# Optimization experiments

Measured on AMD Instinct MI355X. Metric: run time of the kernel, lower is better.

The kernel has to match this reference:

```python
import jax, jax.numpy as jnp
import numpy as np

BATCH, SEQ = 1, 2048
D_MODEL, N_HEADS, D_HEAD = 2048, 16, 128
ROTARY_DIM = 128
N_CTX = 2048
EPS = 1e-5
IGNORE = -100000.0
ATTN_SCALE = float(np.sqrt(D_HEAD))  # use_attn_scale=True, no layer-idx scaling
ROTARY_BASE = 10000.0


def _ln_pre(x):
    # LayerNormPre: center and normalize, no learned scale/bias
    x = x - x.mean(axis=-1, keepdims=True)
    scale = jnp.sqrt((x * x).mean(axis=-1, keepdims=True) + EPS)
    return x / scale


def _sin_cos_rotary(rotary_dim, n_ctx, base=ROTARY_BASE):
    pos = jnp.arange(n_ctx, dtype=jnp.float32)
    dim = jnp.arange(rotary_dim // 2, dtype=jnp.float32)
    freq = base ** (dim / (rotary_dim / 2))
    freq = jnp.repeat(freq, 2)  # einops.repeat 'd -> (d 2)' (interleaved)
    angles = pos[:, None] / freq[None, :]  # [n_ctx, rotary_dim]
    return jnp.sin(angles), jnp.cos(angles)


def _rotate_every_two(x):
    x1 = x[..., 0::2]
    x2 = x[..., 1::2]
    return jnp.stack([-x2, x1], axis=-1).reshape(x.shape)


def _apply_rotary(x, sin, cos):
    # x: [batch, pos, head, d_head]
    n_pos = x.shape[1]
    x_rot = x[..., :ROTARY_DIM]
    x_pass = x[..., ROTARY_DIM:]
    c = cos[:n_pos][:, None, :]  # [pos, 1, rotary_dim] broadcasts over head
    s = sin[:n_pos][:, None, :]
    x_rotated = x_rot * c + _rotate_every_two(x_rot) * s
    return jnp.concatenate([x_rotated, x_pass], axis=-1)


def setup_inputs() -> dict:
    key = jax.random.key(0)
    ks = jax.random.split(key, 6)
    init_std = 0.02
    return {
        "resid_pre": jax.random.normal(ks[0], (BATCH, SEQ, D_MODEL), jnp.float32),
        "W_Q": jax.random.normal(ks[1], (N_HEADS, D_MODEL, D_HEAD), jnp.float32) * init_std,
        "W_K": jax.random.normal(ks[2], (N_HEADS, D_MODEL, D_HEAD), jnp.float32) * init_std,
        "W_V": jax.random.normal(ks[3], (N_HEADS, D_MODEL, D_HEAD), jnp.float32) * init_std,
        "W_O": jax.random.normal(ks[4], (N_HEADS, D_HEAD, D_MODEL), jnp.float32) * init_std,
        "b_Q": jnp.zeros((N_HEADS, D_HEAD), jnp.float32),
        "b_K": jnp.zeros((N_HEADS, D_HEAD), jnp.float32),
        "b_V": jnp.zeros((N_HEADS, D_HEAD), jnp.float32),
        "b_O": jnp.zeros((D_MODEL,), jnp.float32),
    }


def reference(resid_pre, W_Q, W_K, W_V, W_O, b_Q, b_K, b_V, b_O):
    sin, cos = _sin_cos_rotary(ROTARY_DIM, N_CTX)
    xn = _ln_pre(resid_pre)  # LayerNormPre applied to resid_pre for q, k, v
    q = jnp.einsum("bpd,hde->bphe", xn, W_Q) + b_Q
    k = jnp.einsum("bpd,hde->bphe", xn, W_K) + b_K
    v = jnp.einsum("bpd,hde->bphe", xn, W_V) + b_V
    q = _apply_rotary(q, sin, cos)
    k = _apply_rotary(k, sin, cos)
    # attn_scores: [batch, head, query_pos, key_pos]
    scores = jnp.einsum("bqhe,bkhe->bhqk", q, k) / ATTN_SCALE
    n_pos = resid_pre.shape[1]
    causal = jnp.tril(jnp.ones((n_pos, n_pos), dtype=bool))
    scores = jnp.where(causal, scores, jnp.float32(IGNORE))
    attn = jax.nn.softmax(scores, axis=-1)
    z = jnp.einsum("bkhe,bhqk->bqhe", v, attn)
    out = jnp.einsum("bqhe,hed->bqd", z, W_O) + b_O
    return out
```

## Files before the change

### kernel.cpp

```cpp
#include <hip/hip_runtime.h>
#include <hip/hip_bf16.h>

#define SEQ    2048
#define DM     2048
#define NH     16
#define DH     128
#define EPS    1e-5f
#define SCALE_INV 0.08838834764831845f
#define SC2LOG    0.12751744995f

typedef unsigned short u16;
typedef u16  u16x4  __attribute__((ext_vector_type(4)));
typedef u16  u16x8  __attribute__((ext_vector_type(8)));
typedef __bf16 bf16x8 __attribute__((ext_vector_type(8)));
typedef float f32x4 __attribute__((ext_vector_type(4)));

__device__ __forceinline__ u16 f2bf(float f) {
    unsigned int u = __builtin_bit_cast(unsigned int, f);
    u += 0x7fffu + ((u >> 16) & 1u);
    return (u16)(u >> 16);
}
__device__ __forceinline__ float bf2f(u16 v) {
    return __builtin_bit_cast(float, (unsigned)v << 16);
}
__device__ __forceinline__ bf16x8 as_bf(u16x8 v) { return __builtin_bit_cast(bf16x8, v); }

__device__ __forceinline__ void gload16(const u16* g, u16* l) {
    __builtin_amdgcn_global_load_lds(
        (const __attribute__((address_space(1))) unsigned int*)g,
        (__attribute__((address_space(3))) unsigned int*)l, 16, 0, 0);
}

#define VMCNT(N) asm volatile("s_waitcnt vmcnt(" #N ")" ::: "memory")
#define LGKMCNT0 asm volatile("s_waitcnt lgkmcnt(0)" ::: "memory")
#define SCHEDBAR __builtin_amdgcn_sched_barrier(0)
#define BARRIER  __builtin_amdgcn_s_barrier()

__global__ void rope_kernel(float2* __restrict__ tab) {
    int i = threadIdx.x;
    int pos = blockIdx.x;
    float freq = powf(10000.f, (float)i * (1.f / 64.f));
    float ang = (float)pos / freq;
    tab[pos * 64 + i] = make_float2(sinf(ang), cosf(ang));
}

__global__ __launch_bounds__(256) void ln_kernel(const float* __restrict__ x,
                                                 u16* __restrict__ xn) {
    int row = blockIdx.x, t = threadIdx.x;
    const float* xr = x + (size_t)row * DM;
    float4 v0 = *(const float4*)(xr + t * 4);
    float4 v1 = *(const float4*)(xr + 1024 + t * 4);
    float s = v0.x + v0.y + v0.z + v0.w + v1.x + v1.y + v1.z + v1.w;
    float q = v0.x*v0.x + v0.y*v0.y + v0.z*v0.z + v0.w*v0.w
            + v1.x*v1.x + v1.y*v1.y + v1.z*v1.z + v1.w*v1.w;
    #pragma unroll
    for (int o = 32; o; o >>= 1) { s += __shfl_xor(s, o); q += __shfl_xor(q, o); }
    __shared__ float ss[4], qq[4];
    if ((t & 63) == 0) { ss[t >> 6] = s; qq[t >> 6] = q; }
    __syncthreads();
    s = ss[0] + ss[1] + ss[2] + ss[3];
    q = qq[0] + qq[1] + qq[2] + qq[3];
    float mean = s * (1.f / DM);
    float var  = q * (1.f / DM) - mean * mean;
    float rstd = rsqrtf(var + EPS);
    u16* orow = xn + (size_t)row * DM;
    u16x4 o0 = { f2bf((v0.x-mean)*rstd), f2bf((v0.y-mean)*rstd),
                 f2bf((v0.z-mean)*rstd), f2bf((v0.w-mean)*rstd) };
    u16x4 o1 = { f2bf((v1.x-mean)*rstd), f2bf((v1.y-mean)*rstd),
                 f2bf((v1.z-mean)*rstd), f2bf((v1.w-mean)*rstd) };
    *(u16x4*)(orow + t * 4) = o0;
    *(u16x4*)(orow + 1024 + t * 4) = o1;
}

__global__ __launch_bounds__(256) void transpose_qkv(const float* __restrict__ WQ,
                                                     const float* __restrict__ WK,
                                                     const float* __restrict__ WV,
                                                     u16* __restrict__ out) {
    int z = blockIdx.z, which = z >> 4, h = z & 15;
    const float* in = ((which == 0) ? WQ : (which == 1) ? WK : WV) + (size_t)h * DM * DH;
    u16* o = out + (size_t)z * DM * DH;
    int r0 = blockIdx.y * 64, c0 = blockIdx.x * 64;
    __shared__ u16 tile[64][65];
    int t = threadIdx.x;
    #pragma unroll
    for (int it = 0; it < 4; ++it) {
        int idx = t + it * 256;
        int rr = idx >> 4, cc = (idx & 15) * 4;
        float4 v = *(const float4*)(in + (size_t)(r0 + rr) * DH + c0 + cc);
        tile[rr][cc+0] = f2bf(v.x); tile[rr][cc+1] = f2bf(v.y);
        tile[rr][cc+2] = f2bf(v.z); tile[rr][cc+3] = f2bf(v.w);
    }
    __syncthreads();
    #pragma unroll
    for (int it = 0; it < 4; ++it) {
        int idx = t + it * 256;
        int oc = idx >> 4, orr = (idx & 15) * 4;
        u16x4 w = { tile[orr+0][oc], tile[orr+1][oc], tile[orr+2][oc], tile[orr+3][oc] };
        *(u16x4*)(o + (size_t)(c0 + oc) * DM + r0 + orr) = w;
    }
}

__global__ __launch_bounds__(256) void transpose_wo(const float* __restrict__ in,
                                                    u16* __restrict__ out) {
    int r0 = blockIdx.y * 64, c0 = blockIdx.x * 64;
    __shared__ u16 tile[64][65];
    int t = threadIdx.x;
    #pragma unroll
    for (int it = 0; it < 4; ++it) {
        int idx = t + it * 256;
        int rr = idx >> 4, cc = (idx & 15) * 4;
        float4 v = *(const float4*)(in + (size_t)(r0 + rr) * DM + c0 + cc);
        tile[rr][cc+0] = f2bf(v.x); tile[rr][cc+1] = f2bf(v.y);
        tile[rr][cc+2] = f2bf(v.z); tile[rr][cc+3] = f2bf(v.w);
    }
    __syncthreads();
    #pragma unroll
    for (int it = 0; it < 4; ++it) {
        int idx = t + it * 256;
        int oc = idx >> 4, orr = (idx & 15) * 4;
        u16x4 w = { tile[orr+0][oc], tile[orr+1][oc], tile[orr+2][oc], tile[orr+3][oc] };
        *(u16x4*)(out + (size_t)(c0 + oc) * DM + r0 + orr) = w;
    }
}

__global__ __launch_bounds__(512, 2) void gemm_qkv(const u16* __restrict__ Xn,
                                                   const u16* __restrict__ Wt,
                                                   const float* __restrict__ bQ,
                                                   const float* __restrict__ bK,
                                                   const float* __restrict__ bV,
                                                   const float2* __restrict__ rope,
                                                   u16* __restrict__ qkv) {
    __shared__ u16 As[2][256 * 64], Bs[2][256 * 64];
    int id = blockIdx.x;
    int swz = (id & 7) * 24 + (id >> 3);
    int bx = swz & 7, by = swz >> 3;
    int m0 = bx * 256, n0 = by * 256;

    int t = threadIdx.x, lane = t & 63, wid = t >> 6;
    int wr = wid >> 2, wc = wid & 3;
    int cl = lane & 15, g = lane >> 4;

    auto stage = [&](int buf, int kt) {
        const u16* xa = Xn + (size_t)kt * 64;
        const u16* xb = Wt + (size_t)kt * 64;
        #pragma unroll
        for (int j = 0; j < 4; ++j) {
            int idx = t + j * 512;
            int row = idx >> 3;
            int slotS = (idx & 7) ^ (row & 7);
            gload16(xa + (size_t)(m0 + row) * DM + slotS * 8, &As[buf][idx * 8]);
            gload16(xb + (size_t)(n0 + row) * DM + slotS * 8, &Bs[buf][idx * 8]);
        }
    };

    f32x4 acc[8][4] = {};
    stage(0, 0);
    VMCNT(0);
    BARRIER;

    for (int kt = 0; kt < 32; ++kt) {
        int p = kt & 1;
        bool more = (kt + 1 < 32);
        bf16x8 bfr[4][2], af[4][2];
        #pragma unroll
        for (int nj = 0; nj < 4; ++nj)
            #pragma unroll
            for (int kk = 0; kk < 2; ++kk) {
                int row = wc * 64 + nj * 16 + cl;
                int s = (kk * 4 + g) ^ (row & 7);
                bfr[nj][kk] = as_bf(*(const u16x8*)&Bs[p][row * 64 + s * 8]);
            }
        #pragma unroll
        for (int mi = 0; mi < 4; ++mi)
            #pragma unroll
            for (int kk = 0; kk < 2; ++kk) {
                int row = wr * 128 + mi * 16 + cl;
                int s = (kk * 4 + g) ^ (row & 7);
                af[mi][kk] = as_bf(*(const u16x8*)&As[p][row * 64 + s * 8]);
            }
        if (more) stage(p ^ 1, kt + 1);
        __builtin_amdgcn_s_setprio(1);
        #pragma unroll
        for (int mi = 0; mi < 4; ++mi)
            #pragma unroll
            for (int nj = 0; nj < 4; ++nj)
                #pragma unroll
                for (int kk = 0; kk < 2; ++kk)
                    acc[mi][nj] = __builtin_amdgcn_mfma_f32_16x16x32_bf16(af[mi][kk], bfr[nj][kk], acc[mi][nj], 0, 0, 0);
        __builtin_amdgcn_s_setprio(0);
        #pragma unroll
        for (int mi = 0; mi < 4; ++mi)
            #pragma unroll
            for (int kk = 0; kk < 2; ++kk) {
                int row = wr * 128 + 64 + mi * 16 + cl;
                int s = (kk * 4 + g) ^ (row & 7);
                af[mi][kk] = as_bf(*(const u16x8*)&As[p][row * 64 + s * 8]);
            }
        __builtin_amdgcn_s_setprio(1);
        #pragma unroll
        for (int mi = 0; mi < 4; ++mi)
            #pragma unroll
            for (int nj = 0; nj < 4; ++nj)
                #pragma unroll
                for (int kk = 0; kk < 2; ++kk)
                    acc[4 + mi][nj] = __builtin_amdgcn_mfma_f32_16x16x32_bf16(af[mi][kk], bfr[nj][kk], acc[4 + mi][nj], 0, 0, 0);
        __builtin_amdgcn_s_setprio(0);
        VMCNT(0);
        SCHEDBAR;
        BARRIER;
    }

    int which = n0 >> 11;
    const float* bias = (which == 0) ? bQ : (which == 1) ? bK : bV;
    #pragma unroll
    for (int i = 0; i < 8; ++i)
        #pragma unroll
        for (int nj = 0; nj < 4; ++nj) {
            int eg = n0 + wc * 64 + nj * 16 + cl;
            int h = (eg >> 7) & 15;
            int e = eg & 127;
            float bb = bias[h * DH + e];
            int p0 = m0 + wr * 128 + i * 16 + g * 4;
            if (which == 2) {
                u16* vbase = qkv + 2ll * NH * SEQ * DH + (size_t)h * DH * SEQ;
                u16x4 o = { f2bf(acc[i][nj][0] + bb), f2bf(acc[i][nj][1] + bb),
                            f2bf(acc[i][nj][2] + bb), f2bf(acc[i][nj][3] + bb) };
                *(u16x4*)(vbase + (size_t)e * SEQ + p0) = o;
            } else {
                u16* outbase = qkv + ((size_t)which * 16 + h) * SEQ * DH;
                #pragma unroll
                for (int r = 0; r < 4; ++r) {
                    int pp = p0 + r;
                    float v = acc[i][nj][r] + bb;
                    float pv = __shfl_xor(v, 1);
                    float2 sc2 = rope[pp * 64 + (e >> 1)];
                    v = (e & 1) ? (v * sc2.y + pv * sc2.x) : (v * sc2.y - pv * sc2.x);
                    outbase[(size_t)pp * DH + e] = f2bf(v);
                }
            }
        }
}

__device__ __forceinline__ int part_prefix(int j) {
    return (j < 16) ? 2 * (j - 8) : (j < 24 ? 16 + 3 * (j - 16) : 40 + 4 * (j - 24));
}

__global__ __launch_bounds__(256) void flash_kernel(const u16* __restrict__ Qg,
                                                    const u16* __restrict__ Kg,
                                                    const u16* __restrict__ Vt,
                                                    u16* __restrict__ Zg,
                                                    u16* __restrict__ pO,
                                                    float2* __restrict__ ml) {
    __shared__ u16 kt[64 * 128];
    __shared__ u16 vt[128 * 64];
    __shared__ unsigned pt32[4 * 16 * 32];
    int h = blockIdx.x;
    int rem = blockIdx.y;
    int j = 31, c = 0;
    #pragma unroll 1
    for (int jj = 31; jj >= 0; --jj) {
        int ncj = (jj >> 3) + 1;
        if (rem < ncj) { j = jj; c = rem; break; }
        rem -= ncj;
    }
    int q0 = j * 64;
    int nc = (j >> 3) + 1;
    bool multi = (nc > 1);
    int kt0 = c * 8;
    int kt1 = min(j, c * 8 + 7);

    int t = threadIdx.x, lane = t & 63, w = t >> 6;
    int cl = lane & 15, g = lane >> 4;
    int qw0 = q0 + w * 16;
    const size_t hs = (size_t)h * SEQ;
    unsigned* ptw = pt32 + w * (16 * 32) + cl * 32;
    int swv = (cl & 7) << 1;

    bf16x8 qf[4];
    #pragma unroll
    for (int st = 0; st < 4; ++st)
        qf[st] = as_bf(*(const u16x8*)(Qg + (hs + qw0 + cl) * DH + st * 32 + g * 8));

    f32x4 acc[8] = {};
    float mrun = -3e38f, lsum = 0.f;

    u16x8 kreg[4], vreg[4];
    auto load_tile = [&](int kv0) {
        #pragma unroll
        for (int jj = 0; jj < 4; ++jj) {
            int idx = t + jj * 256;
            kreg[jj] = *(const u16x8*)(Kg + (hs + kv0 + (idx >> 4)) * DH + (idx & 15) * 8);
            vreg[jj] = *(const u16x8*)(Vt + ((size_t)h * DH + (idx >> 3)) * SEQ + kv0 + (idx & 7) * 8);
        }
    };
    auto store_tile = [&]() {
        #pragma unroll
        for (int jj = 0; jj < 4; ++jj) {
            int idx = t + jj * 256;
            int row = idx >> 4, slot = idx & 15;
            *(u16x8*)((char*)kt + row * 256 + ((slot ^ (row & 7)) * 16)) = kreg[jj];
            int e = idx >> 3, ch = idx & 7;
            *(u16x8*)((char*)vt + e * 128 + ((ch ^ (e & 7)) * 16)) = vreg[jj];
        }
    };

    int kvbeg = kt0 * 64, kvend = kt1 * 64;
    load_tile(kvbeg);
    store_tile();

    for (int kv0 = kvbeg; kv0 <= kvend; kv0 += 64) {
        __syncthreads();
        bool more = (kv0 + 64 <= kvend);
        if (more) load_tile(kv0 + 64);

        f32x4 sc[4] = {};
        __builtin_amdgcn_s_setprio(1);
        #pragma unroll
        for (int st = 0; st < 4; ++st)
            #pragma unroll
            for (int cc = 0; cc < 4; ++cc) {
                int row = cc * 16 + cl;
                bf16x8 kf = as_bf(*(const u16x8*)((char*)kt + row * 256 + (((st * 4 + g) ^ (row & 7)) * 16)));
                sc[cc] = __builtin_amdgcn_mfma_f32_16x16x32_bf16(kf, qf[st], sc[cc], 0, 0, 0);
            }
        __builtin_amdgcn_s_setprio(0);

        bool needmask = (kv0 + 63 > qw0);
        int qrow = qw0 + cl;
        float pf[4][4];
        float tm = -3e38f;
        #pragma unroll
        for (int cc = 0; cc < 4; ++cc)
            #pragma unroll
            for (int r = 0; r < 4; ++r) {
                int kvq = kv0 + cc * 16 + g * 4 + r;
                float sval = sc[cc][r] * SC2LOG;
                if (needmask) sval = (kvq <= qrow) ? sval : -3e38f;
                pf[cc][r] = sval;
                tm = fmaxf(tm, sval);
            }
        tm = fmaxf(tm, __shfl_xor(tm, 16));
        tm = fmaxf(tm, __shfl_xor(tm, 32));

        if (!__all(tm <= mrun + 12.f)) {
            float mn = fmaxf(mrun, tm);
            float alpha = exp2f(mrun - mn);
            mrun = mn;
            lsum *= alpha;
            float aR[4];
            #pragma unroll
            for (int r = 0; r < 4; ++r) aR[r] = __shfl(alpha, g * 4 + r);
            #pragma unroll
            for (int n = 0; n < 8; ++n)
                #pragma unroll
                for (int r = 0; r < 4; ++r) acc[n][r] *= aR[r];
        }
        float rs = 0.f;
        #pragma unroll
        for (int cc = 0; cc < 4; ++cc)
            #pragma unroll
            for (int r = 0; r < 4; ++r) {
                float e2 = exp2f(pf[cc][r] - mrun);
                pf[cc][r] = e2;
                rs += e2;
            }
        rs += __shfl_xor(rs, 16);
        rs += __shfl_xor(rs, 32);
        lsum += rs;

        #pragma unroll
        for (int cc = 0; cc < 4; ++cc) {
            unsigned lo = (unsigned)f2bf(pf[cc][0]) | ((unsigned)f2bf(pf[cc][1]) << 16);
            unsigned hi = (unsigned)f2bf(pf[cc][2]) | ((unsigned)f2bf(pf[cc][3]) << 16);
            int u = (cc * 4 + g) ^ swv;
            *(unsigned long long*)(ptw + u * 2) =
                (unsigned long long)lo | ((unsigned long long)hi << 32);
        }
        bf16x8 pa[2];
        #pragma unroll
        for (int ks = 0; ks < 2; ++ks)
            pa[ks] = as_bf(*(const u16x8*)(ptw + ((ks * 8 + g * 2) ^ swv) * 2));

        __builtin_amdgcn_s_setprio(1);
        #pragma unroll
        for (int n = 0; n < 8; ++n)
            #pragma unroll
            for (int ks = 0; ks < 2; ++ks) {
                int e = n * 16 + cl;
                bf16x8 vf = as_bf(*(const u16x8*)((char*)vt + e * 128 + (((ks * 4 + g) ^ (e & 7)) * 16)));
                acc[n] = __builtin_amdgcn_mfma_f32_16x16x32_bf16(pa[ks], vf, acc[n], 0, 0, 0);
            }
        __builtin_amdgcn_s_setprio(0);

        if (!more) break;
        __syncthreads();
        store_tile();
    }

    if (multi) {
        int pidx = h * 72 + part_prefix(j) + c;
        if (lane < 16) ml[(size_t)pidx * 64 + w * 16 + cl] = make_float2(mrun, lsum);
        u16* po = pO + (size_t)pidx * (64 * 128);
        #pragma unroll
        for (int n = 0; n < 8; ++n)
            #pragma unroll
            for (int r = 0; r < 4; ++r)
                po[(w * 16 + g * 4 + r) * 128 + n * 16 + cl] = f2bf(acc[n][r]);
    } else {
        float inv = 1.0f / lsum;
        float invR[4];
        #pragma unroll
        for (int r = 0; r < 4; ++r) invR[r] = __shfl(inv, g * 4 + r);
        #pragma unroll
        for (int n = 0; n < 8; ++n)
            #pragma unroll
            for (int r = 0; r < 4; ++r) {
                int q = qw0 + g * 4 + r;
                Zg[(hs + q) * DH + n * 16 + cl] = f2bf(acc[n][r] * invR[r]);
            }
    }
}

__global__ __launch_bounds__(256) void merge_kernel(const u16* __restrict__ pO,
                                                    const float2* __restrict__ ml,
                                                    u16* __restrict__ Zg) {
    int h = blockIdx.x;
    int j = blockIdx.y + 8;
    int nc = (j >> 3) + 1;
    int pbase = h * 72 + part_prefix(j);
    int t = threadIdx.x;
    int row = t >> 2;
    int c0 = (t & 3) * 32;

    float mv[4], lv[4];
    float M = -3e38f;
    #pragma unroll
    for (int i = 0; i < 4; ++i) {
        int ii = (i < nc) ? i : 0;
        float2 mli = ml[(size_t)(pbase + ii) * 64 + row];
        mv[i] = mli.x; lv[i] = mli.y;
        if (i < nc) M = fmaxf(M, mli.x);
    }
    float wgt[4];
    float L = 0.f;
    #pragma unroll
    for (int i = 0; i < 4; ++i) {
        wgt[i] = (i < nc) ? exp2f(mv[i] - M) : 0.f;
        L += wgt[i] * lv[i];
    }
    float invL = 1.f / L;

    #pragma unroll
    for (int ccc = 0; ccc < 32; ccc += 8) {
        float o[8] = {};
        #pragma unroll
        for (int i = 0; i < 4; ++i) {
            int ii = (i < nc) ? i : 0;
            u16x8 v = *(const u16x8*)(pO + ((size_t)(pbase + ii) * 64 + row) * 128 + c0 + ccc);
            #pragma unroll
            for (int k = 0; k < 8; ++k) o[k] += wgt[i] * bf2f(v[k]);
        }
        u16x8 zv;
        #pragma unroll
        for (int k = 0; k < 8; ++k) zv[k] = f2bf(o[k] * invL);
        *(u16x8*)(Zg + ((size_t)h * SEQ + j * 64 + row) * DH + c0 + ccc) = zv;
    }
}

__global__ __launch_bounds__(256) void gemm_out(const u16* __restrict__ Z,
                                                const u16* __restrict__ Wot,
                                                const float* __restrict__ bO,
                                                float* __restrict__ out) {
    __shared__ u16 As[2 * 128 * 32], Bs[2 * 128 * 32];
    int m0 = blockIdx.x * 128, n0 = blockIdx.y * 128;
    int t = threadIdx.x, lane = t & 63, w = t >> 6;
    int wr = w >> 1, wc = w & 1;
    int cl = lane & 15, g = lane >> 4;
    int swz = (cl >> 1) & 3;

    auto stage = [&](int buf, int k0) {
        u16* Ab = As + buf * (128 * 32);
        u16* Bb = Bs + buf * (128 * 32);
        int hh = k0 >> 7, e0 = k0 & 127;
        #pragma unroll
        for (int j = 0; j < 2; ++j) {
            int idx = t + j * 256;
            int row = idx >> 2, slot = idx & 3;
            int slotS = slot ^ ((row >> 1) & 3);
            gload16(Z + ((size_t)hh * SEQ + m0 + row) * DH + e0 + slotS * 8, Ab + idx * 8);
            gload16(Wot + (size_t)(n0 + row) * DM + k0 + slotS * 8, Bb + idx * 8);
        }
    };

    f32x4 acc[4][4] = {};
    stage(0, 0);
    int cur = 0;
    for (int k0 = 0; k0 < DM; k0 += 32) {
        bool more = (k0 + 32 < DM);
        if (more) {
            stage(cur ^ 1, k0 + 32);
            VMCNT(4);
        } else {
            VMCNT(0);
        }
        SCHEDBAR;
        BARRIER;
        const u16* Ac = As + cur * (128 * 32);
        const u16* Bc = Bs + cur * (128 * 32);
        bf16x8 af[4], bfr[4];
        #pragma unroll
        for (int i = 0; i < 4; ++i)
            af[i] = as_bf(*(const u16x8*)&Ac[(wr*64 + i*16 + cl) * 32 + (g ^ swz) * 8]);
        #pragma unroll
        for (int j = 0; j < 4; ++j)
            bfr[j] = as_bf(*(const u16x8*)&Bc[(wc*64 + j*16 + cl) * 32 + (g ^ swz) * 8]);
        #pragma unroll
        for (int i = 0; i < 4; ++i)
            #pragma unroll
            for (int j = 0; j < 4; ++j)
                acc[i][j] = __builtin_amdgcn_mfma_f32_16x16x32_bf16(af[i], bfr[j], acc[i][j], 0, 0, 0);
        LGKMCNT0;
        SCHEDBAR;
        BARRIER;
        cur ^= 1;
    }
    #pragma unroll
    for (int i = 0; i < 4; ++i)
        #pragma unroll
        for (int j = 0; j < 4; ++j) {
            int col = n0 + wc * 64 + j * 16 + cl;
            float bb = bO[col];
            #pragma unroll
            for (int r = 0; r < 4; ++r) {
                int p = m0 + wr * 64 + i * 16 + g * 4 + r;
                out[(size_t)p * DM + col] = acc[i][j][r] + bb;
            }
        }
}

extern "C" void kernel_launch(void* const* d_in, const int* in_sizes, int n_in,
                              void* d_out, int out_size, void* d_ws, size_t ws_size,
                              hipStream_t stream) {
    const float* resid = (const float*)d_in[0];
    const float* WQ = (const float*)d_in[1];
    const float* WK = (const float*)d_in[2];
    const float* WV = (const float*)d_in[3];
    const float* WO = (const float*)d_in[4];
    const float* bQ = (const float*)d_in[5];
    const float* bK = (const float*)d_in[6];
    const float* bV = (const float*)d_in[7];
    const float* bO = (const float*)d_in[8];
    float* out = (float*)d_out;
    char* ws = (char*)d_ws;

    float2* rope = (float2*)(ws);
    u16* xn   = (u16*)(ws + (1ll  << 20));
    u16* Wt   = (u16*)(ws + (9ll  << 20));
    u16* Wot  = (u16*)(ws + (33ll << 20));
    u16* qkv  = (u16*)(ws + (41ll << 20));
    u16* z    = (u16*)(ws + (65ll << 20));
    u16* pO   = (u16*)(ws);
    float2* ml = (float2*)(ws + (20ll << 20));

    rope_kernel<<<SEQ, 64, 0, stream>>>(rope);
    ln_kernel<<<SEQ, 256, 0, stream>>>(resid, xn);

    transpose_qkv<<<dim3(2, 32, 48), 256, 0, stream>>>(WQ, WK, WV, Wt);
    transpose_wo<<<dim3(32, 32, 1), 256, 0, stream>>>(WO, Wot);

    gemm_qkv<<<192, 512, 0, stream>>>(xn, Wt, bQ, bK, bV, rope, qkv);

    const u16* Qg = qkv;
    const u16* Kg = qkv + 1ll * NH * SEQ * DH;
    const u16* Vt = qkv + 2ll * NH * SEQ * DH;
    flash_kernel<<<dim3(NH, 80), 256, 0, stream>>>(Qg, Kg, Vt, z, pO, ml);
    merge_kernel<<<dim3(NH, 24), 256, 0, stream>>>(pO, ml, z);

    gemm_out<<<dim3(16, 16), 256, 0, stream>>>(z, Wot, bO, out);
}
```

Baseline: 201.0 us.

## Restructure output GEMM with BK=64 tiles, early-issued prefetch and block swizzle

Rewrites the output projection GEMM to use 64-wide K tiles with an 8-slot XOR LDS swizzle, halving the number of barrier-synchronised iterations. Fragments are read from LDS first, then the next tile's global loads are issued so they overlap the MFMA block, and MFMA runs at raised wave priority. A 1D grid with a block-index remap groups tiles for L2 reuse of weights and activations. LDS usage doubles to 64KB per block, which may limit occupancy despite the launch_bounds hint.

Measured after the change: 188.8 us. 1.06x faster.

```diff
diff --git a/kernel.cpp b/kernel.cpp
--- a/kernel.cpp
+++ b/kernel.cpp
@@ -467,62 +467,61 @@
     }
 }
 
-__global__ __launch_bounds__(256) void gemm_out(const u16* __restrict__ Z,
-                                                const u16* __restrict__ Wot,
-                                                const float* __restrict__ bO,
-                                                float* __restrict__ out) {
-    __shared__ u16 As[2 * 128 * 32], Bs[2 * 128 * 32];
-    int m0 = blockIdx.x * 128, n0 = blockIdx.y * 128;
+__global__ __launch_bounds__(256, 2) void gemm_out(const u16* __restrict__ Z,
+                                                   const u16* __restrict__ Wot,
+                                                   const float* __restrict__ bO,
+                                                   float* __restrict__ out) {
+    __shared__ u16 As[2][128 * 64], Bs[2][128 * 64];
+    int id = blockIdx.x;
+    int swz = (id & 7) * 32 + (id >> 3);
+    int m0 = (swz & 15) * 128, n0 = (swz >> 4) * 128;
     int t = threadIdx.x, lane = t & 63, w = t >> 6;
     int wr = w >> 1, wc = w & 1;
     int cl = lane & 15, g = lane >> 4;
-    int swz = (cl >> 1) & 3;
-
-    auto stage = [&](int buf, int k0) {
-        u16* Ab = As + buf * (128 * 32);
-        u16* Bb = Bs + buf * (128 * 32);
+
+    auto stage = [&](int buf, int kt) {
+        int k0 = kt * 64;
         int hh = k0 >> 7, e0 = k0 & 127;
         #pragma unroll
-        for (int j = 0; j < 2; ++j) {
+        for (int j = 0; j < 4; ++j) {
             int idx = t + j * 256;
-            int row = idx >> 2, slot = idx & 3;
-            int slotS = slot ^ ((row >> 1) & 3);
-            gload16(Z + ((size_t)hh * SEQ + m0 + row) * DH + e0 + slotS * 8, Ab + idx * 8);
-            gload16(Wot + (size_t)(n0 + row) * DM + k0 + slotS * 8, Bb + idx * 8);
+            int row = idx >> 3;
+            int slotS = (idx & 7) ^ (row & 7);
+            gload16(Z + ((size_t)hh * SEQ + m0 + row) * DH + e0 + slotS * 8, &As[buf][idx * 8]);
+            gload16(Wot + (size_t)(n0 + row) * DM + k0 + slotS * 8, &Bs[buf][idx * 8]);
         }
     };
 
     f32x4 acc[4][4] = {};
     stage(0, 0);
-    int cur = 0;
-    for (int k0 = 0; k0 < DM; k0 += 32) {
-        bool more = (k0 + 32 < DM);
-        if (more) {
-            stage(cur ^ 1, k0 + 32);
-            VMCNT(4);
-        } else {
-            VMCNT(0);
-        }
+    VMCNT(0);
+    BARRIER;
+    for (int kt = 0; kt < 32; ++kt) {
+        int p = kt & 1;
+        bool more = (kt + 1 < 32);
+        bf16x8 af[4][2], bfr[4][2];
+        #pragma unroll
+        for (int i = 0; i < 4; ++i)
+            #pragma unroll
+            for (int kk = 0; kk < 2; ++kk) {
+                int rowA = wr * 64 + i * 16 + cl;
+                af[i][kk] = as_bf(*(const u16x8*)&As[p][rowA * 64 + (((kk * 4 + g) ^ (rowA & 7)) * 8)]);
+                int rowB = wc * 64 + i * 16 + cl;
+                bfr[i][kk] = as_bf(*(const u16x8*)&Bs[p][rowB * 64 + (((kk * 4 + g) ^ (rowB & 7)) * 8)]);
+            }
+        if (more) stage(p ^ 1, kt + 1);
+        __builtin_amdgcn_s_setprio(1);
+        #pragma unroll
+        for (int i = 0; i < 4; ++i)
+            #pragma unroll
+            for (int j = 0; j < 4; ++j)
+                #pragma unroll
+                for (int kk = 0; kk < 2; ++kk)
+                    acc[i][j] = __builtin_amdgcn_mfma_f32_16x16x32_bf16(af[i][kk], bfr[j][kk], acc[i][j], 0, 0, 0);
+        __builtin_amdgcn_s_setprio(0);
+        VMCNT(0);
         SCHEDBAR;
         BARRIER;
-        const u16* Ac = As + cur * (128 * 32);
-        const u16* Bc = Bs + cur * (128 * 32);
-        bf16x8 af[4], bfr[4];
-        #pragma unroll
-        for (int i = 0; i < 4; ++i)
-            af[i] = as_bf(*(const u16x8*)&Ac[(wr*64 + i*16 + cl) * 32 + (g ^ swz) * 8]);
-        #pragma unroll
-        for (int j = 0; j < 4; ++j)
-            bfr[j] = as_bf(*(const u16x8*)&Bc[(wc*64 + j*16 + cl) * 32 + (g ^ swz) * 8]);
-        #pragma unroll
-        for (int i = 0; i < 4; ++i)
-            #pragma unroll
-            for (int j = 0; j < 4; ++j)
-                acc[i][j] = __builtin_amdgcn_mfma_f32_16x16x32_bf16(af[i], bfr[j], acc[i][j], 0, 0, 0);
-        LGKMCNT0;
-        SCHEDBAR;
-        BARRIER;
-        cur ^= 1;
     }
     #pragma unroll
     for (int i = 0; i < 4; ++i)
@@ -576,5 +575,5 @@
     flash_kernel<<<dim3(NH, 80), 256, 0, stream>>>(Qg, Kg, Vt, z, pO, ml);
     merge_kernel<<<dim3(NH, 24), 256, 0, stream>>>(pO, ml, z);
 
-    gemm_out<<<dim3(16, 16), 256, 0, stream>>>(z, Wot, bO, out);
-}
+    gemm_out<<<256, 256, 0, stream>>>(z, Wot, bO, out);
+}
```
